# Kernel optimization log

Hardware: AMD Instinct MI355X
Metric: run time of the kernel (lower is better)

The kernel has to match this reference:

```python
import jax, jax.numpy as jnp
import numpy as np

B, NV, FD = 16, 128, 8192
T_TEMP = 0.2      # self.T
MARGIN = 1.0      # nn.TripletMarginLoss default
EPS = 1e-6        # pairwise_distance eps


def _l2norm(x):
    # torch F.normalize(dim=1): x / max(||x||, 1e-12)
    nrm = jnp.maximum(jnp.linalg.norm(x, axis=-1, keepdims=True), 1e-12)
    return x / nrm


def _ssl_parts(qb, kb, nb, num_gt):
    # qb,kb,nb: [NV, FD] flattened reid embeddings for one image
    qv = _l2norm(qb)[:num_gt]          # [g, FD]
    kv = _l2norm(kb)[:num_gt]          # [g, FD]
    nv = _l2norm(nb)                   # [NV, FD] (negatives are NOT sliced)
    g = num_gt
    S = qv @ kv.T                      # [g, g] all pairwise dots (replaces torch.dot loops)
    # similarity-matrix loss
    sm = jnp.sum((S - jnp.eye(g, dtype=S.dtype)) ** 2) / (g * g)
    # pairwise distances with torch eps convention: ||a - b + eps||_2
    # = sqrt(||a||^2 + ||b||^2 - 2 a.b + 2*eps*(sum(a)-sum(b)) + D*eps^2); ||a||=||b||=1
    sq = qv.sum(axis=1)                # [g]
    sk = kv.sum(axis=1)                # [g]
    const = FD * EPS * EPS
    d_qk = jnp.sqrt(jnp.maximum(2.0 - 2.0 * S + 2.0 * EPS * (sq[:, None] - sk[None, :]) + const, 0.0))
    d_kq = jnp.sqrt(jnp.maximum(2.0 - 2.0 * S.T + 2.0 * EPS * (sk[:, None] - sq[None, :]) + const, 0.0))
    off = 1.0 - jnp.eye(g, dtype=S.dtype)
    # triplet: anc=q_i,pos=k_i,neg=k_j  and  anc=k_i,pos=q_i,neg=q_j, j != i
    tri1 = jnp.sum(jax.nn.relu(jnp.diag(d_qk)[:, None] - d_qk + MARGIN) * off)
    tri2 = jnp.sum(jax.nn.relu(jnp.diag(d_kq)[:, None] - d_kq + MARGIN) * off)
    tri_sum = tri1 + tri2
    # cycle consistency: |q_i.k_j - k_i.q_j| = |S[i,j] - S[j,i]|
    cyc = jnp.sum(jnp.abs(S - S.T) * off) / (g * (g - 1))
    # InfoNCE: l_pos = q_i.k_i, l_neg = q @ n.T
    l_pos = jnp.diag(S)[:, None]       # [g, 1]
    l_neg = qv @ nv.T                  # [g, NV]
    logits = jnp.concatenate([l_pos, l_neg], axis=1) / T_TEMP
    ce = jnp.mean(jax.nn.logsumexp(logits, axis=1) - logits[:, 0])  # CE with labels=0
    return sm, tri_sum, cyc, ce / g


def setup_inputs() -> dict:
    key = jax.random.key(0)
    kq, kk, kn = jax.random.split(key, 3)
    q = jax.random.normal(kq, (B, NV, FD), dtype=jnp.float32)
    k = jax.random.normal(kk, (B, NV, FD), dtype=jnp.float32)
    n = jax.random.normal(kn, (B, NV, FD), dtype=jnp.float32)
    return {"q": q, "k": k, "n": n, "num_gt": NV}


def reference(q, k, n, num_gt):
    sm, tri, cyc, ce = jax.vmap(lambda a, b, c: _ssl_parts(a, b, c, num_gt))(q, k, n)
    tri_cnt = 2 * num_gt * (num_gt - 1)
    # original bug: tri_loss accumulates across batches while tri_cnt resets,
    # so each batch contributes cumsum(tri)[b] / tri_cnt
    ssl = jnp.sum(sm) + jnp.sum(jnp.cumsum(tri)) / tri_cnt + jnp.sum(cyc) + jnp.sum(ce)
    return ssl
```

## Files before the change

### kernel.cpp

```cpp
#include <hip/hip_runtime.h>
#include <cstdint>
#include <cstddef>

#define B_N   16
#define G_N   128
#define FD_N  8192
#define KSPLIT 16
#define KC    512
#define BK2   32
#define NITER 16

typedef unsigned short u16;
typedef u16  u16x4 __attribute__((ext_vector_type(4)));
typedef u16  u16x8 __attribute__((ext_vector_type(8)));
typedef __bf16 bf16x8 __attribute__((ext_vector_type(8)));
typedef float f32x16 __attribute__((ext_vector_type(16)));

#define QSUM_P   0
#define QSSQ_P   32768
#define KSUM_P   65536
#define KSSQ_P   98304
#define NSSQ_P   131072
#define SM_ROW   163840
#define CE_ROW   165888
#define S_OFF    167936
#define PART_OFF_F 430080

__device__ __forceinline__ u16 f2bf(float f) {
    uint32_t u = __float_as_uint(f);
    u += 0x7FFFu + ((u >> 16) & 1u);
    return (u16)(u >> 16);
}

#define LDS_BARRIER() asm volatile("s_waitcnt lgkmcnt(0)\n\ts_barrier" ::: "memory")

__global__ __launch_bounds__(512, 4)
void k_gemm(const float* __restrict__ q, const float* __restrict__ kM,
            const float* __restrict__ nM, float* __restrict__ ws)
{
    __shared__ __align__(16) u16 sA[G_N * BK2];
    __shared__ __align__(16) u16 sB[G_N * BK2];

    const int tid = threadIdx.x;
    const int blk = blockIdx.x;
    const int b    = blk >> 5;
    const int rem  = blk & 31;
    const int half = rem >> 4;
    const int kch  = rem & 15;

    const int r0 = tid >> 3;
    const int c8 = tid & 7;

    const size_t mat_off = (size_t)b * (G_N * FD_N) + (size_t)kch * KC + (size_t)(c8 * 4);
    const float* Ap = q + mat_off;
    const float* Bp = (half ? nM : kM) + mat_off;

    float4 a0[2], b0[2], a1[2], b1[2];
    float aS[2] = {0,0}, aQ[2] = {0,0}, bS[2] = {0,0}, bQ[2] = {0,0};

    #pragma unroll
    for (int i = 0; i < 2; ++i) {
        size_t ro = (size_t)(r0 + 64*i) * FD_N;
        a0[i] = *(const float4*)(Ap + ro);
        b0[i] = *(const float4*)(Bp + ro);
    }
    #pragma unroll
    for (int i = 0; i < 2; ++i) {
        size_t ro = (size_t)(r0 + 64*i) * FD_N + BK2;
        a1[i] = *(const float4*)(Ap + ro);
        b1[i] = *(const float4*)(Bp + ro);
    }

    const int lane  = tid & 63;
    const int wv    = tid >> 6;
    const int wm    = wv >> 2;
    const int wn    = wv & 3;
    const int khalf = lane >> 5;
    const int lrow  = lane & 31;
    const int rA0 = wm*64 + lrow;
    const int rB0 = wn*32 + lrow;

    int wof[2];
    #pragma unroll
    for (int i = 0; i < 2; ++i) {
        int row = r0 + 64*i;
        wof[i] = row*BK2 + 8*((c8>>1) ^ ((row>>1)&3)) + 4*(c8&1);
    }

    f32x16 acc[2];
    #pragma unroll
    for (int mb = 0; mb < 2; ++mb)
      #pragma unroll
      for (int e = 0; e < 16; ++e) acc[mb][e] = 0.f;

#define STORE_STAGE(AR, BR)                                                   \
    {                                                                         \
        _Pragma("unroll")                                                     \
        for (int i = 0; i < 2; ++i) {                                         \
            float4 v = AR[i];                                                 \
            aS[i] += v.x + v.y + v.z + v.w;                                   \
            aQ[i] += v.x*v.x + v.y*v.y + v.z*v.z + v.w*v.w;                   \
            u16x4 h; h[0]=f2bf(v.x); h[1]=f2bf(v.y); h[2]=f2bf(v.z); h[3]=f2bf(v.w); \
            *(u16x4*)(sA + wof[i]) = h;                                       \
            v = BR[i];                                                        \
            bS[i] += v.x + v.y + v.z + v.w;                                   \
            bQ[i] += v.x*v.x + v.y*v.y + v.z*v.z + v.w*v.w;                   \
            u16x4 h2; h2[0]=f2bf(v.x); h2[1]=f2bf(v.y); h2[2]=f2bf(v.z); h2[3]=f2bf(v.w); \
            *(u16x4*)(sB + wof[i]) = h2;                                      \
        }                                                                     \
    }

#define REFILL(AR, BR, KOFF)                                                  \
    {                                                                         \
        _Pragma("unroll")                                                     \
        for (int i = 0; i < 2; ++i) {                                         \
            size_t ro = (size_t)(r0 + 64*i) * FD_N + (KOFF);                  \
            AR[i] = *(const float4*)(Ap + ro);                                \
            BR[i] = *(const float4*)(Bp + ro);                                \
        }                                                                     \
    }

#define MFMA_PHASE()                                                          \
    {                                                                         \
        _Pragma("unroll")                                                     \
        for (int s = 0; s < 2; ++s) {                                         \
            int chunk = s*2 + khalf;                                          \
            bf16x8 af0, af1, bfv;                                             \
            { int row = rA0;                                                  \
              u16x8 raw = *(const u16x8*)(sA + row*BK2 + 8*(chunk ^ ((row>>1)&3))); \
              af0 = __builtin_bit_cast(bf16x8, raw); }                        \
            { int row = rA0 + 32;                                             \
              u16x8 raw = *(const u16x8*)(sA + row*BK2 + 8*(chunk ^ ((row>>1)&3))); \
              af1 = __builtin_bit_cast(bf16x8, raw); }                        \
            { int row = rB0;                                                  \
              u16x8 raw = *(const u16x8*)(sB + row*BK2 + 8*(chunk ^ ((row>>1)&3))); \
              bfv = __builtin_bit_cast(bf16x8, raw); }                        \
            acc[0] = __builtin_amdgcn_mfma_f32_32x32x16_bf16(af0, bfv, acc[0], 0, 0, 0); \
            acc[1] = __builtin_amdgcn_mfma_f32_32x32x16_bf16(af1, bfv, acc[1], 0, 0, 0); \
        }                                                                     \
    }

    for (int kb = 0; kb < NITER; kb += 2) {
        LDS_BARRIER();
        STORE_STAGE(a0, b0);
        LDS_BARRIER();
        if (kb + 2 < NITER) REFILL(a0, b0, (size_t)(kb+2)*BK2);
        MFMA_PHASE();
        LDS_BARRIER();
        STORE_STAGE(a1, b1);
        LDS_BARRIER();
        if (kb + 3 < NITER) REFILL(a1, b1, (size_t)(kb+3)*BK2);
        MFMA_PHASE();
    }

    u16* part = (u16*)(ws + PART_OFF_F) + ((size_t)blk << 14);
    #pragma unroll
    for (int mb = 0; mb < 2; ++mb) {
        int col = wn*32 + lrow;
        int rbase = wm*64 + mb*32 + 4*khalf;
        #pragma unroll
        for (int reg = 0; reg < 16; ++reg) {
            int row = rbase + (reg & 3) + 8*(reg >> 2);
            part[row*G_N + col] = f2bf(acc[mb][reg]);
        }
    }

    #pragma unroll
    for (int i = 0; i < 2; ++i) {
        float sa = aS[i], qa = aQ[i], sb = bS[i], qb = bQ[i];
        #pragma unroll
        for (int m = 4; m >= 1; m >>= 1) {
            sa += __shfl_xor(sa, m, 64); qa += __shfl_xor(qa, m, 64);
            sb += __shfl_xor(sb, m, 64); qb += __shfl_xor(qb, m, 64);
        }
        if (c8 == 0) {
            int o = kch*2048 + b*G_N + (r0 + 64*i);
            if (half == 0) {
                ws[QSUM_P + o] = sa; ws[QSSQ_P + o] = qa;
                ws[KSUM_P + o] = sb; ws[KSSQ_P + o] = qb;
            } else {
                ws[NSSQ_P + o] = qb;
            }
        }
    }
}

__global__ __launch_bounds__(256)
void k_red2(float* __restrict__ ws, float* __restrict__ out)
{
    const int blk  = blockIdx.x;
    const int b    = blk >> 4;
    const int half = (blk >> 3) & 1;
    const int rg   = blk & 7;
    const int t    = threadIdx.x;
    const int lr   = t >> 4;
    const int i    = rg*16 + lr;
    const int c8   = t & 15;
    __shared__ float nrm[128];
    __shared__ float invq_s[16];

    if (blk == 0 && t == 0) out[0] = 0.f;

    if (t < 128) {
        float ss = 0.f;
        const float* p = ws + (half ? NSSQ_P : KSSQ_P) + b*G_N + t;
        #pragma unroll
        for (int kc2 = 0; kc2 < KSPLIT; ++kc2) ss += p[kc2*2048];
        nrm[t] = 1.f / fmaxf(sqrtf(ss), 1e-12f);
    } else if (t < 144) {
        float ss = 0.f;
        const float* p = ws + QSSQ_P + b*G_N + rg*16 + (t - 128);
        #pragma unroll
        for (int kc2 = 0; kc2 < KSPLIT; ++kc2) ss += p[kc2*2048];
        invq_s[t-128] = 1.f / fmaxf(sqrtf(ss), 1e-12f);
    }
    __syncthreads();

    const u16* part = (const u16*)(ws + PART_OFF_F);
    float s[8] = {0,0,0,0,0,0,0,0};
    #pragma unroll
    for (int kc2 = 0; kc2 < KSPLIT; ++kc2) {
        size_t idx = ((size_t)(b*32 + half*16 + kc2) << 14) + i*G_N + c8*8;
        u16x8 h = *(const u16x8*)(part + idx);
        #pragma unroll
        for (int e = 0; e < 8; ++e)
            s[e] += __uint_as_float(((uint32_t)h[e]) << 16);
    }
    const float iq = invq_s[lr];
    if (half == 0) {
        float smacc = 0.f;
        float S8[8];
        #pragma unroll
        for (int e = 0; e < 8; ++e) {
            int j = c8*8 + e;
            S8[e] = s[e] * iq * nrm[j];
            float d = S8[e] - (j == i ? 1.f : 0.f);
            smacc += d*d;
        }
        float* Sp = ws + S_OFF + (size_t)b*16384 + i*G_N + c8*8;
        float4 w0 = {S8[0],S8[1],S8[2],S8[3]};
        float4 w1 = {S8[4],S8[5],S8[6],S8[7]};
        *(float4*)Sp = w0; *(float4*)(Sp+4) = w1;
        #pragma unroll
        for (int m = 8; m >= 1; m >>= 1) smacc += __shfl_xor(smacc, m, 64);
        if (c8 == 0) ws[SM_ROW + b*G_N + i] = smacc;
    } else {
        float eacc = 0.f;
        #pragma unroll
        for (int e = 0; e < 8; ++e)
            eacc += __expf(5.f * s[e] * iq * nrm[c8*8+e]);
        #pragma unroll
        for (int m = 8; m >= 1; m >>= 1) eacc += __shfl_xor(eacc, m, 64);
        if (c8 == 0) ws[CE_ROW + b*G_N + i] = eacc;
    }
}

__global__ __launch_bounds__(256)
void k_epi(float* __restrict__ ws, float* __restrict__ out)
{
    const int blk = blockIdx.x;
    const int b   = blk >> 3;
    const int i0  = (blk & 7) * 16;
    const int t   = threadIdx.x;
    __shared__ float sqv[128], skv[128], ddq[128], ddk[128];
    __shared__ float rbuf[4];
    const float c0 = (float)FD_N * 1e-6f * 1e-6f;

    const float* S = ws + S_OFF + (size_t)b * 16384;
    if (t < 128) {
        float qs=0, qq=0, ks=0, kq=0;
        #pragma unroll
        for (int kc2 = 0; kc2 < KSPLIT; ++kc2) {
            int o = kc2*2048 + b*G_N + t;
            qs += ws[QSUM_P + o]; qq += ws[QSSQ_P + o];
            ks += ws[KSUM_P + o]; kq += ws[KSSQ_P + o];
        }
        float iq = 1.f/fmaxf(sqrtf(qq),1e-12f);
        float ik = 1.f/fmaxf(sqrtf(kq),1e-12f);
        float sq = qs*iq, sk = ks*ik;
        sqv[t]=sq; skv[t]=sk;
        float Stt = S[t*G_N + t];
        ddq[t] = sqrtf(fmaxf(2.f - 2.f*Stt + 2e-6f*(sq-sk) + c0, 0.f));
        ddk[t] = sqrtf(fmaxf(2.f - 2.f*Stt + 2e-6f*(sk-sq) + c0, 0.f));
    }
    __syncthreads();

    float tri=0.f, cyc=0.f, ce=0.f, sm=0.f;
    #pragma unroll
    for (int p = 0; p < 8; ++p) {
        int idx = p*256 + t;
        int i = i0 + (idx >> 7), j = idx & 127;
        if (i != j) {
            float S_ij = S[i*G_N + j];
            float dqk = sqrtf(fmaxf(2.f - 2.f*S_ij + 2e-6f*(sqv[i]-skv[j]) + c0, 0.f));
            tri += fmaxf(ddq[i] - dqk + 1.f, 0.f);
            float dkq = sqrtf(fmaxf(2.f - 2.f*S_ij + 2e-6f*(skv[j]-sqv[i]) + c0, 0.f));
            tri += fmaxf(ddk[j] - dkq + 1.f, 0.f);
            cyc += fabsf(S_ij - S[j*G_N + i]);
        }
    }
    if (t < 16) {
        int r = i0 + t;
        float lp = 5.f * S[r*G_N + r];
        ce = __logf(ws[CE_ROW + b*G_N + r] + __expf(lp)) - lp;
        sm = ws[SM_ROW + b*G_N + r];
    }
    float contrib = sm * (1.f/16384.f) + cyc * (1.f/16256.f) + ce * (1.f/16384.f)
                  + (float)(B_N - b) * tri * (1.f/32512.f);
    #pragma unroll
    for (int m = 32; m >= 1; m >>= 1) contrib += __shfl_xor(contrib, m, 64);
    if ((t & 63) == 0) rbuf[t >> 6] = contrib;
    __syncthreads();
    if (t == 0) atomicAdd(out, rbuf[0] + rbuf[1] + rbuf[2] + rbuf[3]);
}

extern "C" void kernel_launch(void* const* d_in, const int* in_sizes, int n_in,
                              void* d_out, int out_size, void* d_ws, size_t ws_size,
                              hipStream_t stream)
{
    const float* q  = (const float*)d_in[0];
    const float* kM = (const float*)d_in[1];
    const float* nM = (const float*)d_in[2];
    float* ws  = (float*)d_ws;
    float* out = (float*)d_out;

    k_gemm<<<B_N * 2 * KSPLIT, 512, 0, stream>>>(q, kM, nM, ws);
    k_red2<<<256, 256, 0, stream>>>(ws, out);
    k_epi<<<128, 256, 0, stream>>>(ws, out);
}
```

Before: 218.6 us.

## Split GEMM blocks by M half and double-buffer LDS with one barrier per stage

Result: no change. 220.6 us (+1.0%).

```diff
diff --git a/kernel.cpp b/kernel.cpp
--- a/kernel.cpp
+++ b/kernel.cpp
@@ -34,58 +34,48 @@
 
 #define LDS_BARRIER() asm volatile("s_waitcnt lgkmcnt(0)\n\ts_barrier" ::: "memory")
 
-__global__ __launch_bounds__(512, 4)
+__global__ __launch_bounds__(256, 4)
 void k_gemm(const float* __restrict__ q, const float* __restrict__ kM,
             const float* __restrict__ nM, float* __restrict__ ws)
 {
-    __shared__ __align__(16) u16 sA[G_N * BK2];
-    __shared__ __align__(16) u16 sB[G_N * BK2];
+    __shared__ __align__(16) u16 sA[2][64 * BK2];
+    __shared__ __align__(16) u16 sB[2][G_N * BK2];
 
     const int tid = threadIdx.x;
     const int blk = blockIdx.x;
-    const int b    = blk >> 5;
-    const int rem  = blk & 31;
-    const int half = rem >> 4;
-    const int kch  = rem & 15;
-
-    const int r0 = tid >> 3;
+    const int kch   = blk & 15;
+    const int mhalf = (blk >> 4) & 1;
+    const int half  = (blk >> 5) & 1;
+    const int b     = blk >> 6;
+
+    const int r  = tid >> 3;
     const int c8 = tid & 7;
 
-    const size_t mat_off = (size_t)b * (G_N * FD_N) + (size_t)kch * KC + (size_t)(c8 * 4);
-    const float* Ap = q + mat_off;
-    const float* Bp = (half ? nM : kM) + mat_off;
-
-    float4 a0[2], b0[2], a1[2], b1[2];
-    float aS[2] = {0,0}, aQ[2] = {0,0}, bS[2] = {0,0}, bQ[2] = {0,0};
-
+    const size_t base = (size_t)b * (G_N * FD_N) + (size_t)kch * KC + (size_t)(c8 * 4);
+    const float* Ap = q + base + (size_t)(mhalf*64 + r) * FD_N;
+    const float* Bp = (half ? nM : kM) + base + (size_t)r * FD_N;
+
+    float4 a0[2], b0[4], a1[2], b1[4];
+    float aS[2] = {0,0}, aQ[2] = {0,0};
+    float bS[4] = {0,0,0,0}, bQ[4] = {0,0,0,0};
+
+    int wofA[2], wofB[4];
     #pragma unroll
     for (int i = 0; i < 2; ++i) {
-        size_t ro = (size_t)(r0 + 64*i) * FD_N;
-        a0[i] = *(const float4*)(Ap + ro);
-        b0[i] = *(const float4*)(Bp + ro);
-    }
-    #pragma unroll
-    for (int i = 0; i < 2; ++i) {
-        size_t ro = (size_t)(r0 + 64*i) * FD_N + BK2;
-        a1[i] = *(const float4*)(Ap + ro);
-        b1[i] = *(const float4*)(Bp + ro);
+        int row = r + 32*i;
+        wofA[i] = row*BK2 + 8*((c8>>1) ^ ((row>>1)&3)) + 4*(c8&1);
+    }
+    #pragma unroll
+    for (int i = 0; i < 4; ++i) {
+        int row = r + 32*i;
+        wofB[i] = row*BK2 + 8*((c8>>1) ^ ((row>>1)&3)) + 4*(c8&1);
     }
 
     const int lane  = tid & 63;
-    const int wv    = tid >> 6;
-    const int wm    = wv >> 2;
-    const int wn    = wv & 3;
+    const int wn    = tid >> 6;
     const int khalf = lane >> 5;
     const int lrow  = lane & 31;
-    const int rA0 = wm*64 + lrow;
-    const int rB0 = wn*32 + lrow;
-
-    int wof[2];
-    #pragma unroll
-    for (int i = 0; i < 2; ++i) {
-        int row = r0 + 64*i;
-        wof[i] = row*BK2 + 8*((c8>>1) ^ ((row>>1)&3)) + 4*(c8&1);
-    }
+    const int rB0   = wn*32 + lrow;
 
     f32x16 acc[2];
     #pragma unroll
@@ -93,7 +83,17 @@
       #pragma unroll
       for (int e = 0; e < 16; ++e) acc[mb][e] = 0.f;
 
-#define STORE_STAGE(AR, BR)                                                   \
+#define REFILL(AR, BR, KOFF)                                                  \
+    {                                                                         \
+        _Pragma("unroll")                                                     \
+        for (int i = 0; i < 2; ++i)                                           \
+            AR[i] = *(const float4*)(Ap + (size_t)(32*i) * FD_N + (KOFF));    \
+        _Pragma("unroll")                                                     \
+        for (int i = 0; i < 4; ++i)                                           \
+            BR[i] = *(const float4*)(Bp + (size_t)(32*i) * FD_N + (KOFF));    \
+    }
+
+#define STORE_STAGE(BUF, AR, BR)                                              \
     {                                                                         \
         _Pragma("unroll")                                                     \
         for (int i = 0; i < 2; ++i) {                                         \
@@ -101,63 +101,62 @@
             aS[i] += v.x + v.y + v.z + v.w;                                   \
             aQ[i] += v.x*v.x + v.y*v.y + v.z*v.z + v.w*v.w;                   \
             u16x4 h; h[0]=f2bf(v.x); h[1]=f2bf(v.y); h[2]=f2bf(v.z); h[3]=f2bf(v.w); \
-            *(u16x4*)(sA + wof[i]) = h;                                       \
-            v = BR[i];                                                        \
+            *(u16x4*)(sA[BUF] + wofA[i]) = h;                                 \
+        }                                                                     \
+        _Pragma("unroll")                                                     \
+        for (int i = 0; i < 4; ++i) {                                         \
+            float4 v = BR[i];                                                 \
             bS[i] += v.x + v.y + v.z + v.w;                                   \
             bQ[i] += v.x*v.x + v.y*v.y + v.z*v.z + v.w*v.w;                   \
-            u16x4 h2; h2[0]=f2bf(v.x); h2[1]=f2bf(v.y); h2[2]=f2bf(v.z); h2[3]=f2bf(v.w); \
-            *(u16x4*)(sB + wof[i]) = h2;                                      \
+            u16x4 h; h[0]=f2bf(v.x); h[1]=f2bf(v.y); h[2]=f2bf(v.z); h[3]=f2bf(v.w); \
+            *(u16x4*)(sB[BUF] + wofB[i]) = h;                                 \
         }                                                                     \
     }
 
-#define REFILL(AR, BR, KOFF)                                                  \
-    {                                                                         \
-        _Pragma("unroll")                                                     \
-        for (int i = 0; i < 2; ++i) {                                         \
-            size_t ro = (size_t)(r0 + 64*i) * FD_N + (KOFF);                  \
-            AR[i] = *(const float4*)(Ap + ro);                                \
-            BR[i] = *(const float4*)(Bp + ro);                                \
-        }                                                                     \
-    }
-
-#define MFMA_PHASE()                                                          \
+#define MFMA_PHASE(BUF)                                                       \
     {                                                                         \
         _Pragma("unroll")                                                     \
         for (int s = 0; s < 2; ++s) {                                         \
             int chunk = s*2 + khalf;                                          \
             bf16x8 af0, af1, bfv;                                             \
-            { int row = rA0;                                                  \
-              u16x8 raw = *(const u16x8*)(sA + row*BK2 + 8*(chunk ^ ((row>>1)&3))); \
+            { int row = lrow;                                                 \
+              u16x8 raw = *(const u16x8*)(sA[BUF] + row*BK2 + 8*(chunk ^ ((row>>1)&3))); \
               af0 = __builtin_bit_cast(bf16x8, raw); }                        \
-            { int row = rA0 + 32;                                             \
-              u16x8 raw = *(const u16x8*)(sA + row*BK2 + 8*(chunk ^ ((row>>1)&3))); \
+            { int row = lrow + 32;                                            \
+              u16x8 raw = *(const u16x8*)(sA[BUF] + row*BK2 + 8*(chunk ^ ((row>>1)&3))); \
               af1 = __builtin_bit_cast(bf16x8, raw); }                        \
             { int row = rB0;                                                  \
-              u16x8 raw = *(const u16x8*)(sB + row*BK2 + 8*(chunk ^ ((row>>1)&3))); \
+              u16x8 raw = *(const u16x8*)(sB[BUF] + row*BK2 + 8*(chunk ^ ((row>>1)&3))); \
               bfv = __builtin_bit_cast(bf16x8, raw); }                        \
             acc[0] = __builtin_amdgcn_mfma_f32_32x32x16_bf16(af0, bfv, acc[0], 0, 0, 0); \
             acc[1] = __builtin_amdgcn_mfma_f32_32x32x16_bf16(af1, bfv, acc[1], 0, 0, 0); \
         }                                                                     \
     }
 
+    REFILL(a0, b0, 0);
+    REFILL(a1, b1, BK2);
+    STORE_STAGE(0, a0, b0);
+    REFILL(a0, b0, 2*BK2);
+    LDS_BARRIER();
+
     for (int kb = 0; kb < NITER; kb += 2) {
+        STORE_STAGE(1, a1, b1);
+        if (kb + 3 < NITER) REFILL(a1, b1, (size_t)(kb+3)*BK2);
+        MFMA_PHASE(0);
         LDS_BARRIER();
-        STORE_STAGE(a0, b0);
+        if (kb + 2 < NITER) {
+            STORE_STAGE(0, a0, b0);
+            if (kb + 4 < NITER) REFILL(a0, b0, (size_t)(kb+4)*BK2);
+        }
+        MFMA_PHASE(1);
         LDS_BARRIER();
-        if (kb + 2 < NITER) REFILL(a0, b0, (size_t)(kb+2)*BK2);
-        MFMA_PHASE();
-        LDS_BARRIER();
-        STORE_STAGE(a1, b1);
-        LDS_BARRIER();
-        if (kb + 3 < NITER) REFILL(a1, b1, (size_t)(kb+3)*BK2);
-        MFMA_PHASE();
-    }
-
-    u16* part = (u16*)(ws + PART_OFF_F) + ((size_t)blk << 14);
+    }
+
+    u16* part = (u16*)(ws + PART_OFF_F) + ((size_t)blk << 13);
     #pragma unroll
     for (int mb = 0; mb < 2; ++mb) {
         int col = wn*32 + lrow;
-        int rbase = wm*64 + mb*32 + 4*khalf;
+        int rbase = mb*32 + 4*khalf;
         #pragma unroll
         for (int reg = 0; reg < 16; ++reg) {
             int row = rbase + (reg & 3) + 8*(reg >> 2);
@@ -167,20 +166,23 @@
 
     #pragma unroll
     for (int i = 0; i < 2; ++i) {
-        float sa = aS[i], qa = aQ[i], sb = bS[i], qb = bQ[i];
-        #pragma unroll
-        for (int m = 4; m >= 1; m >>= 1) {
-            sa += __shfl_xor(sa, m, 64); qa += __shfl_xor(qa, m, 64);
-            sb += __shfl_xor(sb, m, 64); qb += __shfl_xor(qb, m, 64);
-        }
-        if (c8 == 0) {
-            int o = kch*2048 + b*G_N + (r0 + 64*i);
-            if (half == 0) {
-                ws[QSUM_P + o] = sa; ws[QSSQ_P + o] = qa;
-                ws[KSUM_P + o] = sb; ws[KSSQ_P + o] = qb;
-            } else {
-                ws[NSSQ_P + o] = qb;
-            }
+        float sa = aS[i], qa = aQ[i];
+        #pragma unroll
+        for (int m = 4; m >= 1; m >>= 1) { sa += __shfl_xor(sa, m, 64); qa += __shfl_xor(qa, m, 64); }
+        if (c8 == 0 && half == 0) {
+            int o = kch*2048 + b*G_N + (mhalf*64 + r + 32*i);
+            ws[QSUM_P + o] = sa; ws[QSSQ_P + o] = qa;
+        }
+    }
+    #pragma unroll
+    for (int i = 0; i < 4; ++i) {
+        float sb = bS[i], qb = bQ[i];
+        #pragma unroll
+        for (int m = 4; m >= 1; m >>= 1) { sb += __shfl_xor(sb, m, 64); qb += __shfl_xor(qb, m, 64); }
+        if (c8 == 0 && mhalf == 0) {
+            int o = kch*2048 + b*G_N + (r + 32*i);
+            if (half == 0) { ws[KSUM_P + o] = sb; ws[KSSQ_P + o] = qb; }
+            else           { ws[NSSQ_P + o] = qb; }
         }
     }
 }
@@ -217,10 +219,13 @@
     __syncthreads();
 
     const u16* part = (const u16*)(ws + PART_OFF_F);
+    const int mh   = i >> 6;
+    const int rloc = i & 63;
     float s[8] = {0,0,0,0,0,0,0,0};
     #pragma unroll
     for (int kc2 = 0; kc2 < KSPLIT; ++kc2) {
-        size_t idx = ((size_t)(b*32 + half*16 + kc2) << 14) + i*G_N + c8*8;
+        int pblk = ((b*2 + half)*2 + mh)*16 + kc2;
+        size_t idx = ((size_t)pblk << 13) + rloc*G_N + c8*8;
         u16x8 h = *(const u16x8*)(part + idx);
         #pragma unroll
         for (int e = 0; e < 8; ++e)
@@ -300,10 +305,10 @@
         }
     }
     if (t < 16) {
-        int r = i0 + t;
-        float lp = 5.f * S[r*G_N + r];
-        ce = __logf(ws[CE_ROW + b*G_N + r] + __expf(lp)) - lp;
-        sm = ws[SM_ROW + b*G_N + r];
+        int rr = i0 + t;
+        float lp = 5.f * S[rr*G_N + rr];
+        ce = __logf(ws[CE_ROW + b*G_N + rr] + __expf(lp)) - lp;
+        sm = ws[SM_ROW + b*G_N + rr];
     }
     float contrib = sm * (1.f/16384.f) + cyc * (1.f/16256.f) + ce * (1.f/16384.f)
                   + (float)(B_N - b) * tri * (1.f/32512.f);
@@ -324,7 +329,7 @@
     float* ws  = (float*)d_ws;
     float* out = (float*)d_out;
 
-    k_gemm<<<B_N * 2 * KSPLIT, 512, 0, stream>>>(q, kM, nM, ws);
+    k_gemm<<<B_N * 2 * 2 * KSPLIT, 256, 0, stream>>>(q, kM, nM, ws);
     k_red2<<<256, 256, 0, stream>>>(ws, out);
     k_epi<<<128, 256, 0, stream>>>(ws, out);
 }
```
